# Optimization experiments

Measured on AMD Instinct MI355X. Metric: run time of the kernel, lower is better.

The kernel has to match this reference:

```python
import jax, jax.numpy as jnp
import numpy as np

B, L, HID = 2, 2048, 1024
H = 16
D = HID // H          # head_dim = 64
LR = 16               # gate low-rank dim
EPS = 1e-5
GLN = 16.0            # gate_logit_normalizer
SCALE = D ** -0.5


def setup_inputs() -> dict:
    key = jax.random.key(0)
    ks = jax.random.split(key, 9)
    s = 0.02
    return {
        "x": jax.random.normal(ks[0], (B, L, HID), jnp.float32),
        "Wq": jax.random.normal(ks[1], (HID, HID), jnp.float32) * s,
        "Wk": jax.random.normal(ks[2], (HID, HID), jnp.float32) * s,
        "Wv": jax.random.normal(ks[3], (HID, HID), jnp.float32) * s,
        "Wg1": jax.random.normal(ks[4], (HID, LR), jnp.float32) * s,
        "Wg2": jax.random.normal(ks[5], (LR, HID), jnp.float32) * s,
        "bg2": jnp.zeros((HID,), jnp.float32),
        "Wg": jax.random.normal(ks[6], (HID, HID), jnp.float32) * s,
        "g_norm_w": jnp.ones((D,), jnp.float32),
        "Wo": jax.random.normal(ks[7], (HID, HID), jnp.float32) * s,
    }


def reference(x, Wq, Wk, Wv, Wg1, Wg2, bg2, Wg, g_norm_w, Wo):
    Bb, Ll, Hid = x.shape
    q = (x @ Wq).reshape(Bb, Ll, H, D)
    k = (x @ Wk).reshape(Bb, Ll, H, D)
    v = (x @ Wv).reshape(Bb, Ll, H, D)
    gk = jax.nn.log_sigmoid(((x @ Wg1) @ Wg2 + bg2)).reshape(Bb, Ll, H, D) / GLN

    def step(S, inp):
        q_t, k_t, v_t, gk_t = inp  # each (B, H, D)
        # S: (B,H,D,D); gate broadcasts over the v-dim (last axis)
        S = jnp.exp(gk_t)[..., None] * S + k_t[..., None] * v_t[..., None, :]
        o_t = jnp.einsum('bhdv,bhd->bhv', S, q_t) * SCALE  # S^T @ q / sqrt(D)
        return S, o_t

    S0 = jnp.zeros((Bb, H, D, D), x.dtype)
    scan_in = tuple(jnp.moveaxis(t, 1, 0) for t in (q, k, v, gk))  # (L,B,H,D)
    S, o = jax.lax.scan(step, S0, scan_in)
    o = jnp.moveaxis(o, 0, 1)  # (B, L, H, D)

    # RMSNorm over head_dim with affine weight
    o = o * jax.lax.rsqrt(jnp.mean(o * o, axis=-1, keepdims=True) + EPS) * g_norm_w
    o = o.reshape(Bb, Ll, Hid)

    # Swish output gate
    g = x @ Wg
    o = o * (g * jax.nn.sigmoid(g))
    o = o @ Wo
    return o, S[:, None]  # last_state: (B,1,H,D,D)
```

## Files before the change

kernel.cpp:

```cpp
#include <hip/hip_runtime.h>
#include <hip/hip_bf16.h>

typedef unsigned short u16;
typedef __attribute__((ext_vector_type(8))) short bf16x8;
typedef __attribute__((ext_vector_type(4))) float f32x4;

#define L_SEQ 2048
#define HID 1024
#define NC 32
#define MTOK 4096
#define GEPS 1e-5f
#define QSCALE 0.125f

__device__ __forceinline__ float bf2f(u16 u){ union{unsigned i; float f;}c; c.i=(unsigned)u<<16; return c.f; }
__device__ __forceinline__ u16 f2bf(float f){ union{__hip_bfloat16 h; u16 u;}c; c.h=__float2bfloat16(f); return c.u; }

__device__ __forceinline__ int swz72(int row, int col){ return row * 72 + (col ^ ((row >> 1) & 24)); }

__device__ __forceinline__ void gload_lds16(const u16* g, u16* l){
  __builtin_amdgcn_global_load_lds((const __attribute__((address_space(1))) void*)g,
                                   (__attribute__((address_space(3))) void*)l, 16, 0, 0);
}

__global__ __launch_bounds__(256) void gla_transpose5(const float* W0, const float* W1,
                                                      const float* W2, const float* W3,
                                                      const float* W4,
                                                      u16* D0, u16* D1, u16* D2, u16* D3, u16* D4){
  const float* W; u16* D;
  switch (blockIdx.z){
    case 0: W = W0; D = D0; break;
    case 1: W = W1; D = D1; break;
    case 2: W = W2; D = D2; break;
    case 3: W = W3; D = D3; break;
    default: W = W4; D = D4; break;
  }
  __shared__ float tile[32][33];
  int tx = threadIdx.x & 31, ty = threadIdx.x >> 5;
  int n0 = blockIdx.x * 32, k0 = blockIdx.y * 32;
  #pragma unroll
  for (int r = ty; r < 32; r += 8)
    tile[r][tx] = W[(size_t)(k0 + r) * HID + n0 + tx];
  __syncthreads();
  #pragma unroll
  for (int r = ty; r < 32; r += 8)
    D[(size_t)(n0 + r) * HID + k0 + tx] = f2bf(tile[tx][r]);
}

__global__ __launch_bounds__(256) void gla_xg1(const float* __restrict__ x,
                                               const float* __restrict__ Wg1,
                                               float* __restrict__ xg1,
                                               u16* __restrict__ xb){
  int lane = threadIdx.x & 63, wid = threadIdx.x >> 6;
  int row = blockIdx.x * 4 + wid;
  const float* xr = x + (size_t)row * HID;
  u16* xbr = xb + (size_t)row * HID;
  float acc[16];
  #pragma unroll
  for (int n = 0; n < 16; n++) acc[n] = 0.f;
  for (int k = lane; k < HID; k += 64){
    float xv = xr[k];
    xbr[k] = f2bf(xv);
    const float4* wr = (const float4*)(Wg1 + (size_t)k * 16);
    float4 w0 = wr[0], w1 = wr[1], w2 = wr[2], w3 = wr[3];
    acc[0]  += xv * w0.x; acc[1]  += xv * w0.y; acc[2]  += xv * w0.z; acc[3]  += xv * w0.w;
    acc[4]  += xv * w1.x; acc[5]  += xv * w1.y; acc[6]  += xv * w1.z; acc[7]  += xv * w1.w;
    acc[8]  += xv * w2.x; acc[9]  += xv * w2.y; acc[10] += xv * w2.z; acc[11] += xv * w2.w;
    acc[12] += xv * w3.x; acc[13] += xv * w3.y; acc[14] += xv * w3.z; acc[15] += xv * w3.w;
  }
  #pragma unroll
  for (int n = 0; n < 16; n++){
    #pragma unroll
    for (int off = 32; off > 0; off >>= 1)
      acc[n] += __shfl_down(acc[n], off, 64);
  }
  if (lane == 0){
    #pragma unroll
    for (int n = 0; n < 16; n++) xg1[(size_t)row * 16 + n] = acc[n];
  }
}

__global__ __launch_bounds__(256) void gla_gkcg(const float* __restrict__ xg1,
                                                const float* __restrict__ Wg2,
                                                const float* __restrict__ bg2,
                                                u16* __restrict__ CG){
  __shared__ float xs[64][16];
  int blk = blockIdx.x;
  int b = blk >> 7, r7 = blk & 127;
  int c = r7 >> 2, q = r7 & 3;
  int col = q * 256 + threadIdx.x;
  int tok0 = b * L_SEQ + c * 64;
  {
    int row = threadIdx.x >> 2, e4 = (threadIdx.x & 3) * 4;
    *(float4*)&xs[row][e4] = *(const float4*)&xg1[(size_t)(tok0 + row) * 16 + e4];
  }
  __syncthreads();
  float w[16];
  #pragma unroll
  for (int r = 0; r < 16; r++) w[r] = Wg2[r * HID + col];
  float bz = bg2[col];
  float cum = 0.f;
  for (int t = 0; t < 64; t++){
    float z = bz;
    #pragma unroll
    for (int r = 0; r < 16; r++) z += xs[t][r] * w[r];
    float ls = fminf(z, 0.f) - log1pf(__expf(-fabsf(z)));
    cum += ls * (1.0f / 16.0f);
    CG[(size_t)(tok0 + t) * HID + col] = f2bf(cum);
  }
}

__global__ __launch_bounds__(512) void gla_gemm_qkvg(const u16* __restrict__ A,
                                                     const u16* __restrict__ Bt,
                                                     u16* __restrict__ C){
  constexpr int NT = HID / 32;
  __shared__ u16 As[2][256 * 32];
  __shared__ u16 Bs[2][128 * 32];
  const int tid = threadIdx.x;
  const int lane = tid & 63, wid = tid >> 6;
  const int wm = wid >> 1, wn = wid & 1;
  const int lr = lane & 15, lk = lane >> 4;
  const int id = blockIdx.x + 16 * blockIdx.y;
  const int nid = (id & 7) * 64 + (id >> 3);
  const int bm = nid & 15, bn = nid >> 4;
  const int srow = tid >> 2;
  const int skw  = ((tid & 3) * 8) ^ ((srow & 3) << 3);
  const u16* Ag = A  + ((size_t)bm * 256 + srow) * HID + skw;
  const u16* Bg = Bt + ((size_t)bn * 128 + srow) * HID + skw;

  f32x4 acc[4][4];
  #pragma unroll
  for (int i = 0; i < 4; i++)
    #pragma unroll
    for (int j = 0; j < 4; j++)
      #pragma unroll
      for (int e = 0; e < 4; e++) acc[i][j][e] = 0.f;

  auto STAGE = [&](int buf, int kt){
    gload_lds16(Ag + kt * 32,                         &As[buf][tid * 8]);
    gload_lds16(Ag + (size_t)128 * HID + kt * 32,     &As[buf][4096 + tid * 8]);
    gload_lds16(Bg + kt * 32,                         &Bs[buf][tid * 8]);
  };

  STAGE(0, 0);
  for (int t = 0; t < NT; ++t){
    const int buf = t & 1;
    if (t + 1 < NT){
      STAGE(buf ^ 1, t + 1);
      asm volatile("s_waitcnt vmcnt(3)\ns_barrier" ::: "memory");
    } else {
      asm volatile("s_waitcnt vmcnt(0)\ns_barrier" ::: "memory");
    }
    bf16x8 af[4], bfr[4];
    #pragma unroll
    for (int m = 0; m < 4; m++){
      int row = wm * 64 + m * 16 + lr;
      af[m] = *(const bf16x8*)&As[buf][(row * 32 + lk * 8) ^ ((row & 3) << 3)];
    }
    #pragma unroll
    for (int n = 0; n < 4; n++){
      int row = wn * 64 + n * 16 + lr;
      bfr[n] = *(const bf16x8*)&Bs[buf][(row * 32 + lk * 8) ^ ((row & 3) << 3)];
    }
    __builtin_amdgcn_s_setprio(1);
    #pragma unroll
    for (int m = 0; m < 4; m++)
      #pragma unroll
      for (int n = 0; n < 4; n++)
        acc[m][n] = __builtin_amdgcn_mfma_f32_16x16x32_bf16(af[m], bfr[n], acc[m][n], 0, 0, 0);
    __builtin_amdgcn_s_setprio(0);
    __builtin_amdgcn_sched_barrier(0);
    asm volatile("s_barrier" ::: "memory");
  }

  #pragma unroll
  for (int i = 0; i < 4; i++)
    #pragma unroll
    for (int j = 0; j < 4; j++){
      int row0 = bm * 256 + wm * 64 + i * 16 + lk * 4;
      int cb   = bn * 128 + wn * 64 + j * 16 + lr;
      int sel  = cb >> 10, col = cb & 1023;
      size_t base = (size_t)sel * ((size_t)MTOK * HID) + (size_t)row0 * HID + col;
      #pragma unroll
      for (int r = 0; r < 4; r++)
        C[base + (size_t)r * HID] = f2bf(acc[i][j][r]);
    }
}

__global__ __launch_bounds__(512) void gla_gemm_out_sk(const u16* __restrict__ A,
                                                       const u16* __restrict__ Bt,
                                                       float* __restrict__ C){
  constexpr int NT = 16;
  __shared__ __align__(16) char smem[128 * 132 * 4];
  u16* stage = (u16*)smem;
  float* red = (float*)smem;
  const int tid = threadIdx.x;
  const int lane = tid & 63, wid = tid >> 6;
  const int kg = wid >> 2;
  const int wq = wid & 3;
  const int wm = wq >> 1, wn = wq & 1;
  const int lr = lane & 15, lk = lane >> 4;
  const int id = blockIdx.x + 32 * blockIdx.y;
  const int nid = (id & 7) * 32 + (id >> 3);
  const int bm = nid & 31, bn = nid >> 5;
  const int srow = tid >> 2;
  const int skw  = ((tid & 3) * 8) ^ ((srow & 3) << 3);
  const u16* Ag0 = A  + ((size_t)bm * 128 + srow) * HID + skw;
  const u16* Bg0 = Bt + ((size_t)bn * 128 + srow) * HID + skw;
  const u16* Ag1 = Ag0 + 512;
  const u16* Bg1 = Bg0 + 512;

  f32x4 acc[4][4];
  #pragma unroll
  for (int i = 0; i < 4; i++)
    #pragma unroll
    for (int j = 0; j < 4; j++)
      #pragma unroll
      for (int e = 0; e < 4; e++) acc[i][j][e] = 0.f;

  auto STAGE = [&](int buf, int kt){
    gload_lds16(Ag0 + kt * 32, stage + (buf * 4 + 0) * 4096 + tid * 8);
    gload_lds16(Bg0 + kt * 32, stage + (buf * 4 + 1) * 4096 + tid * 8);
    gload_lds16(Ag1 + kt * 32, stage + (buf * 4 + 2) * 4096 + tid * 8);
    gload_lds16(Bg1 + kt * 32, stage + (buf * 4 + 3) * 4096 + tid * 8);
  };

  STAGE(0, 0);
  for (int t = 0; t < NT; ++t){
    const int buf = t & 1;
    if (t + 1 < NT){
      STAGE(buf ^ 1, t + 1);
      asm volatile("s_waitcnt vmcnt(4)\ns_barrier" ::: "memory");
    } else {
      asm volatile("s_waitcnt vmcnt(0)\ns_barrier" ::: "memory");
    }
    const u16* Ab = stage + (buf * 4 + kg * 2 + 0) * 4096;
    const u16* Bb = stage + (buf * 4 + kg * 2 + 1) * 4096;
    bf16x8 af[4], bfr[4];
    #pragma unroll
    for (int m = 0; m < 4; m++){
      int row = wm * 64 + m * 16 + lr;
      af[m] = *(const bf16x8*)&Ab[(row * 32 + lk * 8) ^ ((row & 3) << 3)];
    }
    #pragma unroll
    for (int n = 0; n < 4; n++){
      int row = wn * 64 + n * 16 + lr;
      bfr[n] = *(const bf16x8*)&Bb[(row * 32 + lk * 8) ^ ((row & 3) << 3)];
    }
    __builtin_amdgcn_s_setprio(1);
    #pragma unroll
    for (int m = 0; m < 4; m++)
      #pragma unroll
      for (int n = 0; n < 4; n++)
        acc[m][n] = __builtin_amdgcn_mfma_f32_16x16x32_bf16(af[m], bfr[n], acc[m][n], 0, 0, 0);
    __builtin_amdgcn_s_setprio(0);
    __builtin_amdgcn_sched_barrier(0);
    asm volatile("s_barrier" ::: "memory");
  }

  if (kg == 1){
    #pragma unroll
    for (int i = 0; i < 4; i++)
      #pragma unroll
      for (int j = 0; j < 4; j++){
        int row = wm * 64 + i * 16 + lk * 4;
        int col = wn * 64 + j * 16 + lr;
        #pragma unroll
        for (int r = 0; r < 4; r++)
          red[(row + r) * 132 + col] = acc[i][j][r];
      }
  }
  __syncthreads();
  if (kg == 0){
    #pragma unroll
    for (int i = 0; i < 4; i++)
      #pragma unroll
      for (int j = 0; j < 4; j++){
        int row = wm * 64 + i * 16 + lk * 4;
        int col = wn * 64 + j * 16 + lr;
        #pragma unroll
        for (int r = 0; r < 4; r++)
          C[(size_t)(bm * 128 + row + r) * HID + bn * 128 + col] =
              acc[i][j][r] + red[(row + r) * 132 + col];
      }
  }
}

__global__ __launch_bounds__(256) void gla_chunk_state2(const u16* __restrict__ Kb,
                                                        const u16* __restrict__ Vb,
                                                        const u16* __restrict__ CG,
                                                        u16* __restrict__ Tbuf,
                                                        float* __restrict__ Dbuf){
  __shared__ u16 KHT[64 * 72];
  __shared__ u16 VT[64 * 72];
  int blk = blockIdx.x;
  int c = blk & (NC - 1), bh = blk >> 5;
  int b = bh >> 4, h = bh & 15;
  int tid = threadIdx.x;
  int lane = tid & 63, w = tid >> 6;
  int lr = lane & 15, lk = lane >> 4;
  int tr = tid >> 2, tc = (tid & 3) * 16;
  size_t gbase = ((size_t)(b * L_SEQ + c * 64)) * HID + h * 64;

  float cg[16], cgl[16];
  {
    const u16* cgp = CG + gbase + (size_t)tr * HID + tc;
    const u16* clp = CG + gbase + (size_t)63 * HID + tc;
    uint4 a0 = *(const uint4*)cgp, a1 = *(const uint4*)(cgp + 8);
    uint4 l0 = *(const uint4*)clp, l1 = *(const uint4*)(clp + 8);
    const u16* au = (const u16*)&a0; const u16* au2 = (const u16*)&a1;
    const u16* lu = (const u16*)&l0; const u16* lu2 = (const u16*)&l1;
    #pragma unroll
    for (int e = 0; e < 8; e++){
      cg[e] = bf2f(au[e]); cg[8 + e] = bf2f(au2[e]);
      cgl[e] = bf2f(lu[e]); cgl[8 + e] = bf2f(lu2[e]);
    }
  }
  {
    const u16* kp = Kb + gbase + (size_t)tr * HID + tc;
    const u16* vp = Vb + gbase + (size_t)tr * HID + tc;
    uint4 kr0 = *(const uint4*)kp, kr1 = *(const uint4*)(kp + 8);
    uint4 vr0 = *(const uint4*)vp, vr1 = *(const uint4*)(vp + 8);
    const u16* ku = (const u16*)&kr0; const u16* ku2 = (const u16*)&kr1;
    const u16* vu = (const u16*)&vr0; const u16* vu2 = (const u16*)&vr1;
    #pragma unroll
    for (int e = 0; e < 8; e++){
      KHT[swz72(tc + e, tr)]     = f2bf(bf2f(ku[e])  * __expf(cgl[e]     - cg[e]));
      KHT[swz72(tc + 8 + e, tr)] = f2bf(bf2f(ku2[e]) * __expf(cgl[8 + e] - cg[8 + e]));
      VT[swz72(tc + e, tr)]      = vu[e];
      VT[swz72(tc + 8 + e, tr)]  = vu2[e];
    }
  }
  if (tr == 0){
    #pragma unroll
    for (int e = 0; e < 16; e++)
      Dbuf[(size_t)blk * 64 + tc + e] = __expf(cgl[e]);
  }
  __syncthreads();
  int R0 = w * 16;
  f32x4 tacc[4];
  #pragma unroll
  for (int v = 0; v < 4; v++)
    #pragma unroll
    for (int e = 0; e < 4; e++) tacc[v][e] = 0.f;
  #pragma unroll
  for (int ks = 0; ks < 2; ks++){
    bf16x8 a = *(const bf16x8*)&KHT[swz72(R0 + lr, ks * 32 + lk * 8)];
    #pragma unroll
    for (int v0 = 0; v0 < 4; v0++){
      bf16x8 bb = *(const bf16x8*)&VT[swz72(v0 * 16 + lr, ks * 32 + lk * 8)];
      tacc[v0] = __builtin_amdgcn_mfma_f32_16x16x32_bf16(a, bb, tacc[v0], 0, 0, 0);
    }
  }
  u16* Tp = Tbuf + (size_t)blk * 4096;
  #pragma unroll
  for (int v0 = 0; v0 < 4; v0++){
    int d = R0 + lk * 4, v = v0 * 16 + lr;
    #pragma unroll
    for (int r = 0; r < 4; r++)
      Tp[(d + r) * 64 + v] = f2bf(tacc[v0][r]);
  }
}

__global__ __launch_bounds__(256) void gla_state_scan2(const u16* __restrict__ Tbuf,
                                                       const float* __restrict__ Dbuf,
                                                       float* __restrict__ Sfin,
                                                       u16* __restrict__ Sinb){
  int bh = blockIdx.x >> 4, seg = blockIdx.x & 15;
  int dv = seg * 256 + threadIdx.x;
  int d = dv >> 6;
  float S = 0.f;
  for (int c = 0; c < NC; c++){
    size_t slot = (size_t)bh * NC + c;
    float t  = bf2f(Tbuf[slot * 4096 + dv]);
    float dec = Dbuf[slot * 64 + d];
    Sinb[slot * 4096 + dv] = f2bf(S);
    S = dec * S + t;
  }
  Sfin[(size_t)bh * 4096 + dv] = S;
}

__global__ __launch_bounds__(256) void gla_chunk_out2(const u16* __restrict__ Qb,
                                                      const u16* __restrict__ Kb,
                                                      const u16* __restrict__ Vb,
                                                      const u16* __restrict__ CG,
                                                      const u16* __restrict__ Sinb,
                                                      const u16* __restrict__ Gb,
                                                      const float* __restrict__ gnw,
                                                      u16* __restrict__ OG){
  __shared__ u16 QT[64 * 72];
  __shared__ u16 KT[64 * 72];
  __shared__ u16 VT[64 * 72];
  __shared__ u16 ST[64 * 72];
  __shared__ u16 PS[64 * 72];
  int blk = blockIdx.x;
  int c = blk & (NC - 1), bh = blk >> 5;
  int b = bh >> 4, h = bh & 15;
  int tid = threadIdx.x;
  int lane = tid & 63, w = tid >> 6;
  int lr = lane & 15, lk = lane >> 4;
  int tr = tid >> 2, tc = (tid & 3) * 16;
  size_t gbase = ((size_t)(b * L_SEQ + c * 64)) * HID + h * 64;

  {
    float cg[16];
    const u16* cgp = CG + gbase + (size_t)tr * HID + tc;
    uint4 a0 = *(const uint4*)cgp, a1 = *(const uint4*)(cgp + 8);
    const u16* au = (const u16*)&a0; const u16* au2 = (const u16*)&a1;
    #pragma unroll
    for (int e = 0; e < 8; e++){ cg[e] = bf2f(au[e]); cg[8 + e] = bf2f(au2[e]); }
    const u16* qp = Qb + gbase + (size_t)tr * HID + tc;
    const u16* kp = Kb + gbase + (size_t)tr * HID + tc;
    const u16* vp = Vb + gbase + (size_t)tr * HID + tc;
    uint4 qr0 = *(const uint4*)qp, qr1 = *(const uint4*)(qp + 8);
    uint4 kr0 = *(const uint4*)kp, kr1 = *(const uint4*)(kp + 8);
    uint4 vr0 = *(const uint4*)vp, vr1 = *(const uint4*)(vp + 8);
    const u16* qu = (const u16*)&qr0; const u16* qu2 = (const u16*)&qr1;
    const u16* ku = (const u16*)&kr0; const u16* ku2 = (const u16*)&kr1;
    const u16* vu = (const u16*)&vr0; const u16* vu2 = (const u16*)&vr1;
    u16 qt[16] __attribute__((aligned(16)));
    u16 kt[16] __attribute__((aligned(16)));
    #pragma unroll
    for (int e = 0; e < 8; e++){
      float ec0 = __expf(cg[e]),  ei0 = __expf(-cg[e]);
      float ec1 = __expf(cg[8+e]), ei1 = __expf(-cg[8+e]);
      qt[e]     = f2bf(bf2f(qu[e])  * ec0 * QSCALE);
      qt[8 + e] = f2bf(bf2f(qu2[e]) * ec1 * QSCALE);
      kt[e]     = f2bf(bf2f(ku[e])  * ei0);
      kt[8 + e] = f2bf(bf2f(ku2[e]) * ei1);
      VT[swz72(tc + e, tr)]     = vu[e];
      VT[swz72(tc + 8 + e, tr)] = vu2[e];
    }
    *(uint4*)&QT[tr * 72 + tc]     = *(uint4*)&qt[0];
    *(uint4*)&QT[tr * 72 + tc + 8] = *(uint4*)&qt[8];
    *(uint4*)&KT[tr * 72 + tc]     = *(uint4*)&kt[0];
    *(uint4*)&KT[tr * 72 + tc + 8] = *(uint4*)&kt[8];
    const u16* sp = Sinb + (size_t)blk * 4096 + (size_t)tr * 64 + tc;
    uint4 s0 = *(const uint4*)sp, s1 = *(const uint4*)(sp + 8);
    const u16* su = (const u16*)&s0; const u16* su2 = (const u16*)&s1;
    #pragma unroll
    for (int e = 0; e < 8; e++){
      ST[swz72(tc + e, tr)]     = su[e];
      ST[swz72(tc + 8 + e, tr)] = su2[e];
    }
  }
  __syncthreads();

  int R0 = w * 16;
  {
    f32x4 pacc[4];
    #pragma unroll
    for (int j = 0; j < 4; j++)
      #pragma unroll
      for (int e = 0; e < 4; e++) pacc[j][e] = 0.f;
    #pragma unroll
    for (int ks = 0; ks < 2; ks++){
      bf16x8 a = *(const bf16x8*)&QT[(R0 + lr) * 72 + ks * 32 + lk * 8];
      #pragma unroll
      for (int j0 = 0; j0 < 4; j0++){
        bf16x8 bb = *(const bf16x8*)&KT[(j0 * 16 + lr) * 72 + ks * 32 + lk * 8];
        pacc[j0] = __builtin_amdgcn_mfma_f32_16x16x32_bf16(a, bb, pacc[j0], 0, 0, 0);
      }
    }
    #pragma unroll
    for (int j0 = 0; j0 < 4; j0++){
      int j = j0 * 16 + lr;
      #pragma unroll
      for (int r = 0; r < 4; r++){
        int t = R0 + lk * 4 + r;
        PS[t * 72 + j] = (j <= t) ? f2bf(pacc[j0][r]) : (u16)0;
      }
    }
  }
  __syncthreads();

  uint4 gr0, gr1;
  {
    const u16* gp = Gb + gbase + (size_t)tr * HID + tc;
    gr0 = *(const uint4*)gp; gr1 = *(const uint4*)(gp + 8);
  }
  f32x4 oacc[4];
  #pragma unroll
  for (int v = 0; v < 4; v++)
    #pragma unroll
    for (int e = 0; e < 4; e++) oacc[v][e] = 0.f;
  #pragma unroll
  for (int ks = 0; ks < 2; ks++){
    bf16x8 a = *(const bf16x8*)&QT[(R0 + lr) * 72 + ks * 32 + lk * 8];
    #pragma unroll
    for (int v0 = 0; v0 < 4; v0++){
      bf16x8 bb = *(const bf16x8*)&ST[swz72(v0 * 16 + lr, ks * 32 + lk * 8)];
      oacc[v0] = __builtin_amdgcn_mfma_f32_16x16x32_bf16(a, bb, oacc[v0], 0, 0, 0);
    }
  }
  #pragma unroll
  for (int ks = 0; ks < 2; ks++){
    bf16x8 a = *(const bf16x8*)&PS[(R0 + lr) * 72 + ks * 32 + lk * 8];
    #pragma unroll
    for (int v0 = 0; v0 < 4; v0++){
      bf16x8 bb = *(const bf16x8*)&VT[swz72(v0 * 16 + lr, ks * 32 + lk * 8)];
      oacc[v0] = __builtin_amdgcn_mfma_f32_16x16x32_bf16(a, bb, oacc[v0], 0, 0, 0);
    }
  }
  *(uint4*)&KT[tr * 72 + tc]     = gr0;
  *(uint4*)&KT[tr * 72 + tc + 8] = gr1;
  __syncthreads();

  {
    float gnv[4];
    #pragma unroll
    for (int v0 = 0; v0 < 4; v0++) gnv[v0] = gnw[v0 * 16 + lr];
    #pragma unroll
    for (int r = 0; r < 4; r++){
      float ssq = 0.f;
      #pragma unroll
      for (int v0 = 0; v0 < 4; v0++) ssq += oacc[v0][r] * oacc[v0][r];
      ssq += __shfl_xor(ssq, 1, 64);
      ssq += __shfl_xor(ssq, 2, 64);
      ssq += __shfl_xor(ssq, 4, 64);
      ssq += __shfl_xor(ssq, 8, 64);
      float rn = rsqrtf(ssq * (1.0f / 64.0f) + GEPS);
      int t = R0 + lk * 4 + r;
      #pragma unroll
      for (int v0 = 0; v0 < 4; v0++){
        float g = bf2f(KT[t * 72 + v0 * 16 + lr]);
        float sw = g / (1.f + __expf(-g));
        ST[swz72(t, v0 * 16 + lr)] = f2bf(oacc[v0][r] * rn * gnv[v0] * sw);
      }
    }
  }
  __syncthreads();
  {
    uint4 o0 = *(uint4*)&ST[swz72(tr, tc)];
    uint4 o1 = *(uint4*)&ST[swz72(tr, tc + 8)];
    u16* op = OG + gbase + (size_t)tr * HID + tc;
    *(uint4*)op       = o0;
    *(uint4*)(op + 8) = o1;
  }
}

extern "C" void kernel_launch(void* const* d_in, const int* in_sizes, int n_in,
                              void* d_out, int out_size, void* d_ws, size_t ws_size,
                              hipStream_t stream){
  (void)in_sizes; (void)n_in; (void)out_size;
  const float* x   = (const float*)d_in[0];
  const float* Wq  = (const float*)d_in[1];
  const float* Wk  = (const float*)d_in[2];
  const float* Wv  = (const float*)d_in[3];
  const float* Wg1 = (const float*)d_in[4];
  const float* Wg2 = (const float*)d_in[5];
  const float* bg2 = (const float*)d_in[6];
  const float* Wg  = (const float*)d_in[7];
  const float* gnw = (const float*)d_in[8];
  const float* Wo  = (const float*)d_in[9];
  float* out = (float*)d_out;

  char* ws = (char*)d_ws;
  size_t off = 0;
  auto alloc = [&](size_t bytes) -> char* {
    char* p = ws + off; off += (bytes + 255) & ~(size_t)255; return p;
  };
  u16* xb   = (u16*)alloc((size_t)MTOK * HID * 2);
  u16* WTq  = (u16*)alloc((size_t)HID * HID * 2);
  u16* WTk  = (u16*)alloc((size_t)HID * HID * 2);
  u16* WTv  = (u16*)alloc((size_t)HID * HID * 2);
  u16* WTg  = (u16*)alloc((size_t)HID * HID * 2);
  u16* WTo  = (u16*)alloc((size_t)HID * HID * 2);
  u16* Qb   = (u16*)alloc((size_t)MTOK * HID * 2);
  u16* Kb   = (u16*)alloc((size_t)MTOK * HID * 2);
  u16* Vb   = (u16*)alloc((size_t)MTOK * HID * 2);
  u16* Gb   = (u16*)alloc((size_t)MTOK * HID * 2);
  u16* CGb  = (u16*)alloc((size_t)MTOK * HID * 2);
  float* xg1b = (float*)alloc((size_t)MTOK * 16 * 4);
  u16* Tbuf = (u16*)alloc((size_t)1024 * 4096 * 2);
  float* Dbuf = (float*)alloc((size_t)1024 * 64 * 4);
  u16* Sinb = (u16*)alloc((size_t)1024 * 4096 * 2);
  u16* OG   = (u16*)alloc((size_t)MTOK * HID * 2);
  if (off > ws_size) return;

  gla_xg1<<<1024, 256, 0, stream>>>(x, Wg1, xg1b, xb);
  dim3 tg(32, 32, 5);
  gla_transpose5<<<tg, 256, 0, stream>>>(Wq, Wk, Wv, Wg, Wo, WTq, WTk, WTv, WTg, WTo);
  gla_gkcg<<<256, 256, 0, stream>>>(xg1b, Wg2, bg2, CGb);

  dim3 gq(16, 32);
  gla_gemm_qkvg<<<gq, 512, 0, stream>>>(xb, WTq, Qb);

  gla_chunk_state2<<<1024, 256, 0, stream>>>(Kb, Vb, CGb, Tbuf, Dbuf);
  gla_state_scan2<<<512, 256, 0, stream>>>(Tbuf, Dbuf, out + (size_t)MTOK * HID, Sinb);
  gla_chunk_out2<<<1024, 256, 0, stream>>>(Qb, Kb, Vb, CGb, Sinb, Gb, gnw, OG);

  dim3 go(32, 8);
  gla_gemm_out_sk<<<go, 512, 0, stream>>>(OG, WTo, out);
}
```

Baseline: 140.3 us.

## Fuse prep kernels, shrink LDS in chunk output, retile output GEMM

Merges the x→bf16/xg1 kernel and the weight-transpose kernel into one launch and vectorises the x loads. Replaces log-sigmoid with a cheaper fast-math form. In the chunk-output kernel, LDS buffers are reused (PS aliased onto KP, ST onto QT with a new swizzle) and the gate is read directly from global memory into registers, which drops one barrier. The output GEMM now uses 64x128 tiles with 256 threads over more blocks, aiming for better occupancy. The new log-sigmoid form can overflow to inf for very negative z, which is a numerical risk.

```diff
diff --git a/kernel.cpp b/kernel.cpp
--- a/kernel.cpp
+++ b/kernel.cpp
@@ -16,66 +16,80 @@
 __device__ __forceinline__ u16 f2bf(float f){ union{__hip_bfloat16 h; u16 u;}c; c.h=__float2bfloat16(f); return c.u; }
 
 __device__ __forceinline__ int swz72(int row, int col){ return row * 72 + (col ^ ((row >> 1) & 24)); }
+__device__ __forceinline__ int swzc(int t){ return ((t >> 2) & 3) << 3; }
 
 __device__ __forceinline__ void gload_lds16(const u16* g, u16* l){
   __builtin_amdgcn_global_load_lds((const __attribute__((address_space(1))) void*)g,
                                    (__attribute__((address_space(3))) void*)l, 16, 0, 0);
 }
 
-__global__ __launch_bounds__(256) void gla_transpose5(const float* W0, const float* W1,
-                                                      const float* W2, const float* W3,
-                                                      const float* W4,
-                                                      u16* D0, u16* D1, u16* D2, u16* D3, u16* D4){
-  const float* W; u16* D;
-  switch (blockIdx.z){
-    case 0: W = W0; D = D0; break;
-    case 1: W = W1; D = D1; break;
-    case 2: W = W2; D = D2; break;
-    case 3: W = W3; D = D3; break;
-    default: W = W4; D = D4; break;
-  }
+__global__ __launch_bounds__(256) void gla_prep(const float* __restrict__ x,
+                                                const float* __restrict__ Wg1,
+                                                float* __restrict__ xg1,
+                                                u16* __restrict__ xb,
+                                                const float* W0, const float* W1,
+                                                const float* W2, const float* W3,
+                                                const float* W4,
+                                                u16* D0, u16* D1, u16* D2, u16* D3, u16* D4){
   __shared__ float tile[32][33];
-  int tx = threadIdx.x & 31, ty = threadIdx.x >> 5;
-  int n0 = blockIdx.x * 32, k0 = blockIdx.y * 32;
-  #pragma unroll
-  for (int r = ty; r < 32; r += 8)
-    tile[r][tx] = W[(size_t)(k0 + r) * HID + n0 + tx];
-  __syncthreads();
-  #pragma unroll
-  for (int r = ty; r < 32; r += 8)
-    D[(size_t)(n0 + r) * HID + k0 + tx] = f2bf(tile[tx][r]);
-}
-
-__global__ __launch_bounds__(256) void gla_xg1(const float* __restrict__ x,
-                                               const float* __restrict__ Wg1,
-                                               float* __restrict__ xg1,
-                                               u16* __restrict__ xb){
-  int lane = threadIdx.x & 63, wid = threadIdx.x >> 6;
-  int row = blockIdx.x * 4 + wid;
-  const float* xr = x + (size_t)row * HID;
-  u16* xbr = xb + (size_t)row * HID;
-  float acc[16];
-  #pragma unroll
-  for (int n = 0; n < 16; n++) acc[n] = 0.f;
-  for (int k = lane; k < HID; k += 64){
-    float xv = xr[k];
-    xbr[k] = f2bf(xv);
-    const float4* wr = (const float4*)(Wg1 + (size_t)k * 16);
-    float4 w0 = wr[0], w1 = wr[1], w2 = wr[2], w3 = wr[3];
-    acc[0]  += xv * w0.x; acc[1]  += xv * w0.y; acc[2]  += xv * w0.z; acc[3]  += xv * w0.w;
-    acc[4]  += xv * w1.x; acc[5]  += xv * w1.y; acc[6]  += xv * w1.z; acc[7]  += xv * w1.w;
-    acc[8]  += xv * w2.x; acc[9]  += xv * w2.y; acc[10] += xv * w2.z; acc[11] += xv * w2.w;
-    acc[12] += xv * w3.x; acc[13] += xv * w3.y; acc[14] += xv * w3.z; acc[15] += xv * w3.w;
-  }
-  #pragma unroll
-  for (int n = 0; n < 16; n++){
-    #pragma unroll
-    for (int off = 32; off > 0; off >>= 1)
-      acc[n] += __shfl_down(acc[n], off, 64);
-  }
-  if (lane == 0){
-    #pragma unroll
-    for (int n = 0; n < 16; n++) xg1[(size_t)row * 16 + n] = acc[n];
+  int bid = blockIdx.x;
+  if (bid < 1024){
+    int lane = threadIdx.x & 63, wid = threadIdx.x >> 6;
+    int row = bid * 4 + wid;
+    const float* xr = x + (size_t)row * HID;
+    u16* xbr = xb + (size_t)row * HID;
+    float acc[16];
+    #pragma unroll
+    for (int n = 0; n < 16; n++) acc[n] = 0.f;
+    #pragma unroll
+    for (int i = 0; i < 4; i++){
+      int k = i * 256 + lane * 4;
+      float4 x4 = *(const float4*)&xr[k];
+      u16 xo[4] __attribute__((aligned(8))) = { f2bf(x4.x), f2bf(x4.y), f2bf(x4.z), f2bf(x4.w) };
+      *(uint2*)&xbr[k] = *(uint2*)xo;
+      const float xv4[4] = { x4.x, x4.y, x4.z, x4.w };
+      #pragma unroll
+      for (int e = 0; e < 4; e++){
+        float xv = xv4[e];
+        const float4* wr = (const float4*)(Wg1 + (size_t)(k + e) * 16);
+        float4 w0 = wr[0], w1 = wr[1], w2 = wr[2], w3 = wr[3];
+        acc[0]  += xv * w0.x; acc[1]  += xv * w0.y; acc[2]  += xv * w0.z; acc[3]  += xv * w0.w;
+        acc[4]  += xv * w1.x; acc[5]  += xv * w1.y; acc[6]  += xv * w1.z; acc[7]  += xv * w1.w;
+        acc[8]  += xv * w2.x; acc[9]  += xv * w2.y; acc[10] += xv * w2.z; acc[11] += xv * w2.w;
+        acc[12] += xv * w3.x; acc[13] += xv * w3.y; acc[14] += xv * w3.z; acc[15] += xv * w3.w;
+      }
+    }
+    #pragma unroll
+    for (int n = 0; n < 16; n++){
+      #pragma unroll
+      for (int off = 32; off > 0; off >>= 1)
+        acc[n] += __shfl_down(acc[n], off, 64);
+    }
+    if (lane == 0){
+      #pragma unroll
+      for (int n = 0; n < 16; n++) xg1[(size_t)row * 16 + n] = acc[n];
+    }
+  } else {
+    int id = bid - 1024;
+    int z = id >> 10, rem = id & 1023;
+    int bx = rem & 31, by = rem >> 5;
+    const float* W; u16* D;
+    switch (z){
+      case 0: W = W0; D = D0; break;
+      case 1: W = W1; D = D1; break;
+      case 2: W = W2; D = D2; break;
+      case 3: W = W3; D = D3; break;
+      default: W = W4; D = D4; break;
+    }
+    int tx = threadIdx.x & 31, ty = threadIdx.x >> 5;
+    int n0 = bx * 32, k0 = by * 32;
+    #pragma unroll
+    for (int r = ty; r < 32; r += 8)
+      tile[r][tx] = W[(size_t)(k0 + r) * HID + n0 + tx];
+    __syncthreads();
+    #pragma unroll
+    for (int r = ty; r < 32; r += 8)
+      D[(size_t)(n0 + r) * HID + k0 + tx] = f2bf(tile[tx][r]);
   }
 }
 
@@ -103,7 +117,7 @@
     float z = bz;
     #pragma unroll
     for (int r = 0; r < 16; r++) z += xs[t][r] * w[r];
-    float ls = fminf(z, 0.f) - log1pf(__expf(-fabsf(z)));
+    float ls = -__logf(1.f + __expf(-z));
     cum += ls * (1.0f / 16.0f);
     CG[(size_t)(tok0 + t) * HID + col] = f2bf(cum);
   }
@@ -186,28 +200,21 @@
     }
 }
 
-__global__ __launch_bounds__(512) void gla_gemm_out_sk(const u16* __restrict__ A,
-                                                       const u16* __restrict__ Bt,
-                                                       float* __restrict__ C){
+__global__ __launch_bounds__(256) void gla_gemm_out2(const u16* __restrict__ A,
+                                                     const u16* __restrict__ Bt,
+                                                     float* __restrict__ C){
   constexpr int NT = 16;
-  __shared__ __align__(16) char smem[128 * 132 * 4];
-  u16* stage = (u16*)smem;
-  float* red = (float*)smem;
+  __shared__ __align__(16) char smem[49152];
   const int tid = threadIdx.x;
   const int lane = tid & 63, wid = tid >> 6;
-  const int kg = wid >> 2;
-  const int wq = wid & 3;
-  const int wm = wq >> 1, wn = wq & 1;
+  const int kg = wid >> 1, w = wid & 1;
   const int lr = lane & 15, lk = lane >> 4;
-  const int id = blockIdx.x + 32 * blockIdx.y;
-  const int nid = (id & 7) * 32 + (id >> 3);
-  const int bm = nid & 31, bn = nid >> 5;
+  const int bm = blockIdx.x, bn = blockIdx.y;
   const int srow = tid >> 2;
   const int skw  = ((tid & 3) * 8) ^ ((srow & 3) << 3);
-  const u16* Ag0 = A  + ((size_t)bm * 128 + srow) * HID + skw;
-  const u16* Bg0 = Bt + ((size_t)bn * 128 + srow) * HID + skw;
-  const u16* Ag1 = Ag0 + 512;
-  const u16* Bg1 = Bg0 + 512;
+  const u16* Ag = A  + ((size_t)bm * 64  + srow) * HID + skw;
+  const u16* Bg = Bt + ((size_t)bn * 128 + srow) * HID + skw;
+  auto seg = [&](int g, int buf) -> u16* { return (u16*)(smem + (g * 2 + buf) * 12288); };
 
   f32x4 acc[4][4];
   #pragma unroll
@@ -218,10 +225,12 @@
       for (int e = 0; e < 4; e++) acc[i][j][e] = 0.f;
 
   auto STAGE = [&](int buf, int kt){
-    gload_lds16(Ag0 + kt * 32, stage + (buf * 4 + 0) * 4096 + tid * 8);
-    gload_lds16(Bg0 + kt * 32, stage + (buf * 4 + 1) * 4096 + tid * 8);
-    gload_lds16(Ag1 + kt * 32, stage + (buf * 4 + 2) * 4096 + tid * 8);
-    gload_lds16(Bg1 + kt * 32, stage + (buf * 4 + 3) * 4096 + tid * 8);
+    gload_lds16(Ag + kt * 32,                          seg(0, buf) + tid * 8);
+    gload_lds16(Bg + kt * 32,                          seg(0, buf) + 2048 + tid * 8);
+    gload_lds16(Bg + (size_t)64 * HID + kt * 32,       seg(0, buf) + 4096 + tid * 8);
+    gload_lds16(Ag + 512 + kt * 32,                    seg(1, buf) + tid * 8);
+    gload_lds16(Bg + 512 + kt * 32,                    seg(1, buf) + 2048 + tid * 8);
+    gload_lds16(Bg + (size_t)64 * HID + 512 + kt * 32, seg(1, buf) + 4096 + tid * 8);
   };
 
   STAGE(0, 0);
@@ -229,21 +238,21 @@
     const int buf = t & 1;
     if (t + 1 < NT){
       STAGE(buf ^ 1, t + 1);
-      asm volatile("s_waitcnt vmcnt(4)\ns_barrier" ::: "memory");
+      asm volatile("s_waitcnt vmcnt(6)\ns_barrier" ::: "memory");
     } else {
       asm volatile("s_waitcnt vmcnt(0)\ns_barrier" ::: "memory");
     }
-    const u16* Ab = stage + (buf * 4 + kg * 2 + 0) * 4096;
-    const u16* Bb = stage + (buf * 4 + kg * 2 + 1) * 4096;
+    const u16* Ab = seg(kg, buf);
+    const u16* Bb = seg(kg, buf) + 2048;
     bf16x8 af[4], bfr[4];
     #pragma unroll
     for (int m = 0; m < 4; m++){
-      int row = wm * 64 + m * 16 + lr;
+      int row = m * 16 + lr;
       af[m] = *(const bf16x8*)&Ab[(row * 32 + lk * 8) ^ ((row & 3) << 3)];
     }
     #pragma unroll
     for (int n = 0; n < 4; n++){
-      int row = wn * 64 + n * 16 + lr;
+      int row = w * 64 + n * 16 + lr;
       bfr[n] = *(const bf16x8*)&Bb[(row * 32 + lk * 8) ^ ((row & 3) << 3)];
     }
     __builtin_amdgcn_s_setprio(1);
@@ -257,30 +266,29 @@
     asm volatile("s_barrier" ::: "memory");
   }
 
+  float* red = (float*)smem;
   if (kg == 1){
     #pragma unroll
-    for (int i = 0; i < 4; i++)
-      #pragma unroll
-      for (int j = 0; j < 4; j++){
-        int row = wm * 64 + i * 16 + lk * 4;
-        int col = wn * 64 + j * 16 + lr;
+    for (int m = 0; m < 4; m++)
+      #pragma unroll
+      for (int n = 0; n < 4; n++){
+        int lrow = m * 16 + lk * 4, lcol = w * 64 + n * 16 + lr;
         #pragma unroll
         for (int r = 0; r < 4; r++)
-          red[(row + r) * 132 + col] = acc[i][j][r];
+          red[(lrow + r) * 132 + lcol] = acc[m][n][r];
       }
   }
   __syncthreads();
   if (kg == 0){
     #pragma unroll
-    for (int i = 0; i < 4; i++)
-      #pragma unroll
-      for (int j = 0; j < 4; j++){
-        int row = wm * 64 + i * 16 + lk * 4;
-        int col = wn * 64 + j * 16 + lr;
+    for (int m = 0; m < 4; m++)
+      #pragma unroll
+      for (int n = 0; n < 4; n++){
+        int lrow = m * 16 + lk * 4, lcol = w * 64 + n * 16 + lr;
         #pragma unroll
         for (int r = 0; r < 4; r++)
-          C[(size_t)(bm * 128 + row + r) * HID + bn * 128 + col] =
-              acc[i][j][r] + red[(row + r) * 132 + col];
+          C[(size_t)(bm * 64 + lrow + r) * HID + bn * 128 + lcol] =
+              acc[m][n][r] + red[(lrow + r) * 132 + lcol];
       }
   }
 }
@@ -388,10 +396,9 @@
                                                       const float* __restrict__ gnw,
                                                       u16* __restrict__ OG){
   __shared__ u16 QT[64 * 72];
-  __shared__ u16 KT[64 * 72];
+  __shared__ u16 KP[64 * 72];
   __shared__ u16 VT[64 * 72];
   __shared__ u16 ST[64 * 72];
-  __shared__ u16 PS[64 * 72];
   int blk = blockIdx.x;
   int c = blk & (NC - 1), bh = blk >> 5;
   int b = bh >> 4, h = bh & 15;
@@ -432,8 +439,8 @@
     }
     *(uint4*)&QT[tr * 72 + tc]     = *(uint4*)&qt[0];
     *(uint4*)&QT[tr * 72 + tc + 8] = *(uint4*)&qt[8];
-    *(uint4*)&KT[tr * 72 + tc]     = *(uint4*)&kt[0];
-    *(uint4*)&KT[tr * 72 + tc + 8] = *(uint4*)&kt[8];
+    *(uint4*)&KP[tr * 72 + tc]     = *(uint4*)&kt[0];
+    *(uint4*)&KP[tr * 72 + tc + 8] = *(uint4*)&kt[8];
     const u16* sp = Sinb + (size_t)blk * 4096 + (size_t)tr * 64 + tc;
     uint4 s0 = *(const uint4*)sp, s1 = *(const uint4*)(sp + 8);
     const u16* su = (const u16*)&s0; const u16* su2 = (const u16*)&s1;
@@ -446,38 +453,32 @@
   __syncthreads();
 
   int R0 = w * 16;
-  {
-    f32x4 pacc[4];
-    #pragma unroll
-    for (int j = 0; j < 4; j++)
-      #pragma unroll
-      for (int e = 0; e < 4; e++) pacc[j][e] = 0.f;
-    #pragma unroll
-    for (int ks = 0; ks < 2; ks++){
-      bf16x8 a = *(const bf16x8*)&QT[(R0 + lr) * 72 + ks * 32 + lk * 8];
-      #pragma unroll
-      for (int j0 = 0; j0 < 4; j0++){
-        bf16x8 bb = *(const bf16x8*)&KT[(j0 * 16 + lr) * 72 + ks * 32 + lk * 8];
-        pacc[j0] = __builtin_amdgcn_mfma_f32_16x16x32_bf16(a, bb, pacc[j0], 0, 0, 0);
-      }
-    }
+  f32x4 pacc[4];
+  #pragma unroll
+  for (int j = 0; j < 4; j++)
+    #pragma unroll
+    for (int e = 0; e < 4; e++) pacc[j][e] = 0.f;
+  #pragma unroll
+  for (int ks = 0; ks < 2; ks++){
+    bf16x8 a = *(const bf16x8*)&QT[(R0 + lr) * 72 + ks * 32 + lk * 8];
     #pragma unroll
     for (int j0 = 0; j0 < 4; j0++){
-      int j = j0 * 16 + lr;
-      #pragma unroll
-      for (int r = 0; r < 4; r++){
-        int t = R0 + lk * 4 + r;
-        PS[t * 72 + j] = (j <= t) ? f2bf(pacc[j0][r]) : (u16)0;
-      }
+      bf16x8 bb = *(const bf16x8*)&KP[(j0 * 16 + lr) * 72 + ks * 32 + lk * 8];
+      pacc[j0] = __builtin_amdgcn_mfma_f32_16x16x32_bf16(a, bb, pacc[j0], 0, 0, 0);
     }
   }
   __syncthreads();
 
-  uint4 gr0, gr1;
-  {
-    const u16* gp = Gb + gbase + (size_t)tr * HID + tc;
-    gr0 = *(const uint4*)gp; gr1 = *(const uint4*)(gp + 8);
-  }
+  #pragma unroll
+  for (int j0 = 0; j0 < 4; j0++){
+    int j = j0 * 16 + lr;
+    #pragma unroll
+    for (int r = 0; r < 4; r++){
+      int t = R0 + lk * 4 + r;
+      KP[t * 72 + (j ^ swzc(t))] = (j <= t) ? f2bf(pacc[j0][r]) : (u16)0;
+    }
+  }
+
   f32x4 oacc[4];
   #pragma unroll
   for (int v = 0; v < 4; v++)
@@ -494,18 +495,24 @@
   }
   #pragma unroll
   for (int ks = 0; ks < 2; ks++){
-    bf16x8 a = *(const bf16x8*)&PS[(R0 + lr) * 72 + ks * 32 + lk * 8];
+    int arow = R0 + lr;
+    bf16x8 a = *(const bf16x8*)&KP[arow * 72 + ((ks * 32 + lk * 8) ^ swzc(arow))];
     #pragma unroll
     for (int v0 = 0; v0 < 4; v0++){
       bf16x8 bb = *(const bf16x8*)&VT[swz72(v0 * 16 + lr, ks * 32 + lk * 8)];
       oacc[v0] = __builtin_amdgcn_mfma_f32_16x16x32_bf16(a, bb, oacc[v0], 0, 0, 0);
     }
   }
-  *(uint4*)&KT[tr * 72 + tc]     = gr0;
-  *(uint4*)&KT[tr * 72 + tc + 8] = gr1;
-  __syncthreads();
 
   {
+    float gv[4][4];
+    #pragma unroll
+    for (int r = 0; r < 4; r++){
+      int t = R0 + lk * 4 + r;
+      #pragma unroll
+      for (int v0 = 0; v0 < 4; v0++)
+        gv[r][v0] = bf2f(Gb[gbase + (size_t)t * HID + v0 * 16 + lr]);
+    }
     float gnv[4];
     #pragma unroll
     for (int v0 = 0; v0 < 4; v0++) gnv[v0] = gnw[v0 * 16 + lr];
@@ -522,16 +529,17 @@
       int t = R0 + lk * 4 + r;
       #pragma unroll
       for (int v0 = 0; v0 < 4; v0++){
-        float g = bf2f(KT[t * 72 + v0 * 16 + lr]);
+        float g = gv[r][v0];
         float sw = g / (1.f + __expf(-g));
-        ST[swz72(t, v0 * 16 + lr)] = f2bf(oacc[v0][r] * rn * gnv[v0] * sw);
+        QT[t * 72 + ((v0 * 16 + lr) ^ swzc(t))] = f2bf(oacc[v0][r] * rn * gnv[v0] * sw);
       }
     }
   }
   __syncthreads();
   {
-    uint4 o0 = *(uint4*)&ST[swz72(tr, tc)];
-    uint4 o1 = *(uint4*)&ST[swz72(tr, tc + 8)];
+    int x0 = swzc(tr);
+    uint4 o0 = *(uint4*)&QT[tr * 72 + (tc ^ x0)];
+    uint4 o1 = *(uint4*)&QT[tr * 72 + ((tc + 8) ^ x0)];
     u16* op = OG + gbase + (size_t)tr * HID + tc;
     *(uint4*)op       = o0;
     *(uint4*)(op + 8) = o1;
@@ -577,9 +585,8 @@
   u16* OG   = (u16*)alloc((size_t)MTOK * HID * 2);
   if (off > ws_size) return;
 
-  gla_xg1<<<1024, 256, 0, stream>>>(x, Wg1, xg1b, xb);
-  dim3 tg(32, 32, 5);
-  gla_transpose5<<<tg, 256, 0, stream>>>(Wq, Wk, Wv, Wg, Wo, WTq, WTk, WTv, WTg, WTo);
+  gla_prep<<<6144, 256, 0, stream>>>(x, Wg1, xg1b, xb, Wq, Wk, Wv, Wg, Wo,
+                                     WTq, WTk, WTv, WTg, WTo);
   gla_gkcg<<<256, 256, 0, stream>>>(xg1b, Wg2, bg2, CGb);
 
   dim3 gq(16, 32);
@@ -589,6 +596,6 @@
   gla_state_scan2<<<512, 256, 0, stream>>>(Tbuf, Dbuf, out + (size_t)MTOK * HID, Sinb);
   gla_chunk_out2<<<1024, 256, 0, stream>>>(Qb, Kb, Vb, CGb, Sinb, Gb, gnw, OG);
 
-  dim3 go(32, 8);
-  gla_gemm_out_sk<<<go, 512, 0, stream>>>(OG, WTo, out);
-}
+  dim3 go(64, 8);
+  gla_gemm_out2<<<go, 256, 0, stream>>>(OG, WTo, out);
+}
```

Result: faster. 135.8 us (-3.2%).
